# Optimization experiments

Measured on AMD Instinct MI355X. Metric: run time of the kernel, lower is better.

Reference implementation:

```python
import jax, jax.numpy as jnp
import numpy as np

HEADS1, HID = 2, 128
OUT_FEATS = 256
K, M = 8, 128


def _gat_conv(x, src, dst, W, a_src, a_dst, bias, heads, out_dim, concat, neg_slope):
    """PyG-style GATConv: linear -> per-edge leakyrelu attention -> dst-softmax -> scatter-sum."""
    N = x.shape[0]
    h = (x @ W.T).reshape(N, heads, out_dim)          # [N, H, D]
    alpha_src = jnp.sum(h * a_src, axis=-1)            # [N, H]
    alpha_dst = jnp.sum(h * a_dst, axis=-1)            # [N, H]
    e = jax.nn.leaky_relu(alpha_src[src] + alpha_dst[dst], neg_slope)  # [E, H]
    # numerically stable segment softmax over incoming edges per destination
    m = jax.ops.segment_max(e, dst, num_segments=N)    # [N, H]
    e = jnp.exp(e - m[dst])
    s = jax.ops.segment_sum(e, dst, num_segments=N)    # [N, H]
    alpha = e / s[dst]                                  # [E, H]
    msg = h[src] * alpha[:, :, None]                    # [E, H, D]
    out = jax.ops.segment_sum(msg, dst, num_segments=N)  # [N, H, D]
    out = out.reshape(N, heads * out_dim) if concat else out.mean(axis=1)
    return out + bias


def setup_inputs() -> dict:
    key = jax.random.key(0)
    ks = jax.random.split(key, 14)
    N, E, IN = 50000, 800000, 256
    x = jax.random.normal(ks[0], (N, IN), dtype=jnp.float32)
    edge_index = jax.random.randint(ks[1], (2, E), 0, N, dtype=jnp.int64)
    sc = 0.1
    return {
        "x": x,
        "edge_index": edge_index,
        "W1": jax.random.normal(ks[2], (HEADS1 * HID, IN), dtype=jnp.float32) * sc,
        "a_src1": jax.random.normal(ks[3], (HEADS1, HID), dtype=jnp.float32) * sc,
        "a_dst1": jax.random.normal(ks[4], (HEADS1, HID), dtype=jnp.float32) * sc,
        "b1": jax.random.normal(ks[5], (HEADS1 * HID,), dtype=jnp.float32) * sc,
        "W2": jax.random.normal(ks[6], (OUT_FEATS, HEADS1 * HID), dtype=jnp.float32) * sc,
        "a_src2": jax.random.normal(ks[7], (1, OUT_FEATS), dtype=jnp.float32) * sc,
        "a_dst2": jax.random.normal(ks[8], (1, OUT_FEATS), dtype=jnp.float32) * sc,
        "b2": jax.random.normal(ks[9], (OUT_FEATS,), dtype=jnp.float32) * sc,
        "g": jax.random.normal(ks[10], (OUT_FEATS, K * M), dtype=jnp.float32) * sc,
        "mu": jax.random.normal(ks[11], (K, M), dtype=jnp.float32) * sc,
    }


def reference(x, edge_index, W1, a_src1, a_dst1, b1, W2, a_src2, a_dst2, b2, g, mu):
    N = x.shape[0]
    loops = jnp.arange(N, dtype=edge_index.dtype)  # PyG GATConv adds self-loops by default
    src = jnp.concatenate([edge_index[0], loops])
    dst = jnp.concatenate([edge_index[1], loops])
    h = _gat_conv(x, src, dst, W1, a_src1, a_dst1, b1, HEADS1, HID, True, 0.2)
    h = jax.nn.leaky_relu(h, 0.01)  # F.leaky_relu default slope
    h = _gat_conv(h, src, dst, W2, a_src2, a_dst2, b2, 1, OUT_FEATS, False, 0.2)
    out = (h @ g).reshape(N, K, M)                      # [N, K, M]
    # cosine similarity against mu along M (torch eps=1e-8)
    num = jnp.einsum('nkm,km->nk', out, mu)
    denom = jnp.maximum(
        jnp.linalg.norm(out, axis=-1) * jnp.linalg.norm(mu, axis=-1)[None, :], 1e-8
    )
    return num / denom  # [N, K]
```

## Files before the change

kernel.cpp:

```cpp
#include <hip/hip_runtime.h>
#include <math.h>

typedef short s16x8 __attribute__((ext_vector_type(8)));
typedef float f32x4 __attribute__((ext_vector_type(4)));

__device__ __forceinline__ float lrelu(float x, float s) { return x > 0.0f ? x : s * x; }

__device__ __forceinline__ unsigned short f2bf(float f) {
  unsigned int u = __float_as_uint(f);
  u = (u + 0x7FFFu + ((u >> 16) & 1u)) >> 16;
  return (unsigned short)u;
}
__device__ __forceinline__ float bf2f(unsigned short h) {
  return __uint_as_float(((unsigned int)h) << 16);
}

__device__ __forceinline__ void gload_lds16(void* lds, const void* g) {
  __builtin_amdgcn_global_load_lds(
      (const __attribute__((address_space(1))) unsigned int*)g,
      (__attribute__((address_space(3))) unsigned int*)lds, 16, 0, 0);
}

__global__ void deg_kernel(const int* __restrict__ dst, int* __restrict__ deg, int E) {
  int e = blockIdx.x * blockDim.x + threadIdx.x;
  if (e < E) atomicAdd(&deg[dst[e]], 1);
}

__global__ __launch_bounds__(256) void bsum_kernel(const int* __restrict__ deg,
                                                   int* __restrict__ bsum, int N) {
  int t = blockIdx.x * 256 + threadIdx.x;
  int v = (t < N) ? deg[t] : 0;
  #pragma unroll
  for (int off = 1; off < 64; off <<= 1) v += __shfl_xor(v, off, 64);
  __shared__ int ws[4];
  if ((threadIdx.x & 63) == 0) ws[threadIdx.x >> 6] = v;
  __syncthreads();
  if (threadIdx.x == 0) bsum[blockIdx.x] = ws[0] + ws[1] + ws[2] + ws[3];
}

__global__ __launch_bounds__(256) void bscan_kernel(const int* __restrict__ bsum,
                                                    int* __restrict__ boff, int nb,
                                                    int* __restrict__ rowptr_total) {
  __shared__ int s[256];
  int t = threadIdx.x;
  int v = (t < nb) ? bsum[t] : 0;
  s[t] = v;
  __syncthreads();
  for (int off = 1; off < 256; off <<= 1) {
    int u = (t >= off) ? s[t - off] : 0;
    __syncthreads();
    s[t] += u;
    __syncthreads();
  }
  if (t < nb) boff[t] = s[t] - v;
  if (t == nb - 1) *rowptr_total = s[t];
}

__global__ __launch_bounds__(256) void bwrite_kernel(const int* __restrict__ deg,
                                                     const int* __restrict__ boff,
                                                     int* __restrict__ rowptr,
                                                     int* __restrict__ cursor, int N) {
  __shared__ int s[256];
  int t = blockIdx.x * 256 + threadIdx.x;
  int v = (t < N) ? deg[t] : 0;
  s[threadIdx.x] = v;
  __syncthreads();
  for (int off = 1; off < 256; off <<= 1) {
    int u = (threadIdx.x >= off) ? s[threadIdx.x - off] : 0;
    __syncthreads();
    s[threadIdx.x] += u;
    __syncthreads();
  }
  if (t < N) {
    int ex = boff[blockIdx.x] + s[threadIdx.x] - v;
    rowptr[t] = ex;
    cursor[t] = ex;
  }
}

__global__ void fill_kernel(const int* __restrict__ src, const int* __restrict__ dst,
                            int* __restrict__ cursor, int* __restrict__ colsrc, int E) {
  int e = blockIdx.x * blockDim.x + threadIdx.x;
  if (e < E) {
    int d = dst[e];
    int pos = atomicAdd(&cursor[d], 1);
    colsrc[pos] = src[e];
  }
}

__global__ void cvt_rows_kernel(const float* __restrict__ src, unsigned short* __restrict__ dst,
                                int nrows, int prows) {
  int t = blockIdx.x * blockDim.x + threadIdx.x;
  int row = t >> 6;
  int c = (t & 63) * 4;
  if (row >= prows) return;
  float4 v = make_float4(0.f, 0.f, 0.f, 0.f);
  if (row < nrows) v = *(const float4*)&src[(size_t)row * 256 + c];
  ushort4 o;
  o.x = f2bf(v.x); o.y = f2bf(v.y); o.z = f2bf(v.z); o.w = f2bf(v.w);
  *(ushort4*)&dst[(size_t)row * 256 + c] = o;
}

__global__ void cvt_gT_kernel(const float* __restrict__ g, unsigned short* __restrict__ gT) {
  int idx = blockIdx.x * blockDim.x + threadIdx.x;
  int k = idx >> 10, n = idx & 1023;
  gT[(size_t)n * 256 + k] = f2bf(g[idx]);
}

template<int EPI, int AH>
__global__ __launch_bounds__(256, 2) void gemm_bf16(
    const unsigned short* __restrict__ A, const unsigned short* __restrict__ B,
    unsigned short* __restrict__ Cb,
    const float* __restrict__ avs, const float* __restrict__ avd,
    float* __restrict__ asrcO, float* __restrict__ adstO,
    const float* __restrict__ mu, const float* __restrict__ nmu,
    float* __restrict__ outcos, int M)
{
  __shared__ unsigned short As[128 * 64];
  __shared__ unsigned short Bs[128 * 64];
  const int t = threadIdx.x;
  const int w = t >> 6;
  const int l = t & 63;
  const int m0 = blockIdx.x * 128;
  const int n0 = blockIdx.y * 128;

  f32x4 acc[2][8];
  #pragma unroll
  for (int i = 0; i < 2; ++i)
    #pragma unroll
    for (int j = 0; j < 8; ++j) acc[i][j] = (f32x4){0.f, 0.f, 0.f, 0.f};

  const unsigned char* Ab = (const unsigned char*)A;
  const unsigned char* Bb = (const unsigned char*)B;
  unsigned char* AsB = (unsigned char*)As;
  unsigned char* BsB = (unsigned char*)Bs;

  const int srow = l >> 3;
  const int gchk = (l & 7) ^ srow;

  for (int kb = 0; kb < 256; kb += 64) {
    #pragma unroll
    for (int i = 0; i < 4; ++i) {
      int seg = w * 4 + i;
      int row = seg * 8 + srow;
      gload_lds16(AsB + seg * 1024,
                  Ab + (size_t)(m0 + row) * 512 + kb * 2 + gchk * 16);
      gload_lds16(BsB + seg * 1024,
                  Bb + (size_t)(n0 + row) * 512 + kb * 2 + gchk * 16);
    }
    asm volatile("s_waitcnt vmcnt(0)" ::: "memory");
    __syncthreads();

    const int rl = l & 15;
    const int kc = l >> 4;
    #pragma unroll
    for (int ks = 0; ks < 2; ++ks) {
      s16x8 af[2], bfr[8];
      #pragma unroll
      for (int mf = 0; mf < 2; ++mf) {
        int r = w * 32 + mf * 16 + rl;
        int slot = (ks * 4 + kc) ^ (r & 7);
        af[mf] = *(const s16x8*)&As[r * 64 + slot * 8];
      }
      #pragma unroll
      for (int nf = 0; nf < 8; ++nf) {
        int r = nf * 16 + rl;
        int slot = (ks * 4 + kc) ^ (r & 7);
        bfr[nf] = *(const s16x8*)&Bs[r * 64 + slot * 8];
      }
      #pragma unroll
      for (int mf = 0; mf < 2; ++mf)
        #pragma unroll
        for (int nf = 0; nf < 8; ++nf)
          acc[mf][nf] = __builtin_amdgcn_mfma_f32_16x16x32_bf16(af[mf], bfr[nf], acc[mf][nf], 0, 0, 0);
    }
    __syncthreads();
  }

  if (EPI == 0) {
    #pragma unroll
    for (int mf = 0; mf < 2; ++mf)
      #pragma unroll
      for (int nf = 0; nf < 8; ++nf)
        #pragma unroll
        for (int j = 0; j < 4; ++j) {
          int r = m0 + w * 32 + mf * 16 + (l >> 4) * 4 + j;
          int c = n0 + nf * 16 + (l & 15);
          Cb[(size_t)r * 256 + c] = f2bf(acc[mf][nf][j]);
        }
    if (AH > 0) {
      float avS[8], avD[8];
      #pragma unroll
      for (int nf = 0; nf < 8; ++nf) {
        avS[nf] = avs[n0 + nf * 16 + (l & 15)];
        avD[nf] = avd[n0 + nf * 16 + (l & 15)];
      }
      #pragma unroll
      for (int mf = 0; mf < 2; ++mf)
        #pragma unroll
        for (int j = 0; j < 4; ++j) {
          float ds = 0.f, dd = 0.f;
          #pragma unroll
          for (int nf = 0; nf < 8; ++nf) {
            float o = acc[mf][nf][j];
            ds = fmaf(o, avS[nf], ds);
            dd = fmaf(o, avD[nf], dd);
          }
          #pragma unroll
          for (int off = 1; off < 16; off <<= 1) {
            ds += __shfl_xor(ds, off, 64);
            dd += __shfl_xor(dd, off, 64);
          }
          if ((l & 15) == 0) {
            int r = m0 + w * 32 + mf * 16 + (l >> 4) * 4 + j;
            if (r < M) {
              if (AH == 2) {
                asrcO[(size_t)r * 2 + blockIdx.y] = ds;
                adstO[(size_t)r * 2 + blockIdx.y] = dd;
              } else {
                atomicAdd(&asrcO[r], ds);
                atomicAdd(&adstO[r], dd);
              }
            }
          }
        }
    }
  } else {
    const int kchunk = blockIdx.y;
    float nm = nmu[kchunk];
    float mv[8];
    #pragma unroll
    for (int nf = 0; nf < 8; ++nf) mv[nf] = mu[kchunk * 128 + nf * 16 + (l & 15)];
    #pragma unroll
    for (int mf = 0; mf < 2; ++mf)
      #pragma unroll
      for (int j = 0; j < 4; ++j) {
        float num = 0.f, ss = 0.f;
        #pragma unroll
        for (int nf = 0; nf < 8; ++nf) {
          float o = acc[mf][nf][j];
          num = fmaf(o, mv[nf], num);
          ss  = fmaf(o, o, ss);
        }
        #pragma unroll
        for (int off = 1; off < 16; off <<= 1) {
          num += __shfl_xor(num, off, 64);
          ss  += __shfl_xor(ss, off, 64);
        }
        if ((l & 15) == 0) {
          int r = m0 + w * 32 + mf * 16 + (l >> 4) * 4 + j;
          if (r < M) outcos[(size_t)r * 8 + kchunk] = num / fmaxf(sqrtf(ss) * nm, 1e-8f);
        }
      }
  }
}

template<int H, bool OUT_LRELU>
__global__ __launch_bounds__(256) void agg_kernel(
    const unsigned short* __restrict__ hin, const float* __restrict__ asrc,
    const float* __restrict__ adst, const int* __restrict__ rowptr,
    const int* __restrict__ colsrc, const float* __restrict__ bias,
    unsigned short* __restrict__ outp, int N)
{
  int wid  = threadIdx.x >> 6;
  int lane = threadIdx.x & 63;
  int n = blockIdx.x * 4 + wid;
  if (n >= N) return;
  const int half = lane >> 5;
  const int fl   = lane & 31;
  const int head = (H == 2) ? (fl >> 4) : 0;

  int beg = rowptr[n], end = rowptr[n + 1];

  float ad0 = adst[(size_t)n * H + 0];
  float ad1 = (H == 2) ? adst[(size_t)n * 2 + 1] : 0.f;
  float m0 = lrelu(asrc[(size_t)n * H + 0] + ad0, 0.2f);
  float m1 = (H == 2) ? lrelu(asrc[(size_t)n * 2 + 1] + ad1, 0.2f) : 0.f;
  float s0 = 1.f, s1 = 1.f;

  float acc[8];
  {
    s16x8 hv = *(const s16x8*)&hin[(size_t)n * 256 + fl * 8];
    #pragma unroll
    for (int k = 0; k < 8; ++k)
      acc[k] = (half == 0) ? bf2f((unsigned short)hv[k]) : 0.f;
  }

  for (int cbeg = beg; cbeg < end; cbeg += 64) {
    int cnt = end - cbeg; if (cnt > 64) cnt = 64;
    int src_i = 0;
    float e0 = -1e30f, e1 = -1e30f;
    if (lane < cnt) {
      src_i = colsrc[cbeg + lane];
      if (H == 2) {
        float2 av = *(const float2*)&asrc[(size_t)src_i * 2];
        e0 = lrelu(av.x + ad0, 0.2f);
        e1 = lrelu(av.y + ad1, 0.2f);
      } else {
        e0 = lrelu(asrc[src_i] + ad0, 0.2f);
      }
    }
    float c0 = e0, c1 = e1;
    #pragma unroll
    for (int off = 32; off >= 1; off >>= 1) {
      c0 = fmaxf(c0, __shfl_xor(c0, off, 64));
      if (H == 2) c1 = fmaxf(c1, __shfl_xor(c1, off, 64));
    }
    float nm0 = fmaxf(m0, c0);
    float r0 = __expf(m0 - nm0); m0 = nm0;
    float r1 = 1.f;
    if (H == 2) { float nm1 = fmaxf(m1, c1); r1 = __expf(m1 - nm1); m1 = nm1; }
    s0 *= r0; if (H == 2) s1 *= r1;
    float rh = (H == 2 && head) ? r1 : r0;
    #pragma unroll
    for (int k = 0; k < 8; ++k) acc[k] *= rh;
    float p0 = (lane < cnt) ? __expf(e0 - m0) : 0.f;
    float p1 = (H == 2 && lane < cnt) ? __expf(e1 - m1) : 0.f;
    float t0 = p0, t1 = p1;
    #pragma unroll
    for (int off = 32; off >= 1; off >>= 1) {
      t0 += __shfl_xor(t0, off, 64);
      if (H == 2) t1 += __shfl_xor(t1, off, 64);
    }
    s0 += t0; if (H == 2) s1 += t1;

    int npair = (cnt + 1) >> 1;
    int pi = 0;
    for (; pi + 2 <= npair; pi += 2) {
      int ia = pi * 2, ib = pi * 2 + 2;
      int sa0 = __shfl(src_i, ia, 64),     sa1 = __shfl(src_i, ia + 1, 64);
      int sb0 = __shfl(src_i, ib, 64),     sb1 = __shfl(src_i, ib + 1, 64);
      float qa00 = __shfl(p0, ia, 64),     qa01 = __shfl(p0, ia + 1, 64);
      float qb00 = __shfl(p0, ib, 64),     qb01 = __shfl(p0, ib + 1, 64);
      float wA, wB;
      if (H == 2) {
        float qa10 = __shfl(p1, ia, 64), qa11 = __shfl(p1, ia + 1, 64);
        float qb10 = __shfl(p1, ib, 64), qb11 = __shfl(p1, ib + 1, 64);
        wA = head ? (half ? qa11 : qa10) : (half ? qa01 : qa00);
        wB = head ? (half ? qb11 : qb10) : (half ? qb01 : qb00);
      } else {
        wA = half ? qa01 : qa00;
        wB = half ? qb01 : qb00;
      }
      int sjA = half ? sa1 : sa0;
      int sjB = half ? sb1 : sb0;
      s16x8 vA = *(const s16x8*)&hin[(size_t)sjA * 256 + fl * 8];
      s16x8 vB = *(const s16x8*)&hin[(size_t)sjB * 256 + fl * 8];
      #pragma unroll
      for (int k = 0; k < 8; ++k) acc[k] = fmaf(bf2f((unsigned short)vA[k]), wA, acc[k]);
      #pragma unroll
      for (int k = 0; k < 8; ++k) acc[k] = fmaf(bf2f((unsigned short)vB[k]), wB, acc[k]);
    }
    for (; pi < npair; ++pi) {
      int ia = pi * 2;
      int sa0 = __shfl(src_i, ia, 64), sa1 = __shfl(src_i, ia + 1, 64);
      float qa00 = __shfl(p0, ia, 64), qa01 = __shfl(p0, ia + 1, 64);
      float wA;
      if (H == 2) {
        float qa10 = __shfl(p1, ia, 64), qa11 = __shfl(p1, ia + 1, 64);
        wA = head ? (half ? qa11 : qa10) : (half ? qa01 : qa00);
      } else {
        wA = half ? qa01 : qa00;
      }
      int sjA = half ? sa1 : sa0;
      s16x8 vA = *(const s16x8*)&hin[(size_t)sjA * 256 + fl * 8];
      #pragma unroll
      for (int k = 0; k < 8; ++k) acc[k] = fmaf(bf2f((unsigned short)vA[k]), wA, acc[k]);
    }
  }

  float sh = (H == 2 && head) ? s1 : s0;
  float inv = 1.0f / sh;
  #pragma unroll
  for (int k = 0; k < 8; ++k) acc[k] += __shfl_xor(acc[k], 32, 64);
  if (half == 0) {
    float bv[8];
    *(float4*)&bv[0] = *(const float4*)&bias[fl * 8];
    *(float4*)&bv[4] = *(const float4*)&bias[fl * 8 + 4];
    s16x8 o;
    #pragma unroll
    for (int k = 0; k < 8; ++k) {
      float v = acc[k] * inv + bv[k];
      if (OUT_LRELU) v = lrelu(v, 0.01f);
      o[k] = (short)f2bf(v);
    }
    *(s16x8*)&outp[(size_t)n * 256 + fl * 8] = o;
  }
}

__global__ __launch_bounds__(64) void munorm_kernel(const float* __restrict__ mu,
                                                    float* __restrict__ norm_mu) {
  int lane = threadIdx.x;
  for (int k = 0; k < 8; ++k) {
    float v0 = mu[k * 128 + lane];
    float v1 = mu[k * 128 + 64 + lane];
    float s = v0 * v0 + v1 * v1;
    #pragma unroll
    for (int off = 1; off < 64; off <<= 1) s += __shfl_xor(s, off, 64);
    if (lane == 0) norm_mu[k] = sqrtf(s);
  }
}

extern "C" void kernel_launch(void* const* d_in, const int* in_sizes, int n_in,
                              void* d_out, int out_size, void* d_ws, size_t ws_size,
                              hipStream_t stream) {
  const float* x      = (const float*)d_in[0];
  const int*   ei     = (const int*)  d_in[1];
  const float* W1     = (const float*)d_in[2];
  const float* a_src1 = (const float*)d_in[3];
  const float* a_dst1 = (const float*)d_in[4];
  const float* b1     = (const float*)d_in[5];
  const float* W2     = (const float*)d_in[6];
  const float* a_src2 = (const float*)d_in[7];
  const float* a_dst2 = (const float*)d_in[8];
  const float* b2     = (const float*)d_in[9];
  const float* g      = (const float*)d_in[10];
  const float* mu     = (const float*)d_in[11];

  const int N  = in_sizes[0] / 256;
  const int E  = in_sizes[1] / 2;
  const int Mp = ((N + 127) / 128) * 128;
  const int nb = (N + 255) / 256;
  const int* src = ei;
  const int* dst = ei + E;

  unsigned short* us = (unsigned short*)d_ws;
  size_t off = 0;
  unsigned short* xb  = us + off; off += (size_t)Mp * 256;
  unsigned short* h1b = us + off; off += (size_t)Mp * 256;
  unsigned short* o1b = us + off; off += (size_t)Mp * 256;
  unsigned short* h2b = us + off; off += (size_t)Mp * 256;
  unsigned short* o2b = xb;
  float* f = (float*)(us + off);
  size_t fo = 0;
  float* asrc1 = f + fo; fo += (size_t)N * 2;
  float* adst1 = f + fo; fo += (size_t)N * 2;
  float* asrc2 = f + fo; fo += N;
  float* adst2 = f + fo; fo += N;
  float* nmu   = f + fo; fo += 8;
  int* deg    = (int*)(f + fo);
  int* rowptr = deg + N;
  int* cursor = rowptr + N + 1;
  int* colsrc = cursor + N;
  int* bsum   = colsrc + E;
  int* boff   = bsum + 256;
  unsigned short* w1b = (unsigned short*)(boff + 256);
  unsigned short* w2b = w1b + 256 * 256;
  unsigned short* gTb = w2b + 256 * 256;

  hipMemsetAsync(deg, 0, (size_t)N * sizeof(int), stream);
  hipMemsetAsync(asrc2, 0, (size_t)N * 2 * sizeof(float), stream);
  deg_kernel<<<(E + 255) / 256, 256, 0, stream>>>(dst, deg, E);
  bsum_kernel<<<nb, 256, 0, stream>>>(deg, bsum, N);
  bscan_kernel<<<1, 256, 0, stream>>>(bsum, boff, nb, rowptr + N);
  bwrite_kernel<<<nb, 256, 0, stream>>>(deg, boff, rowptr, cursor, N);
  fill_kernel<<<(E + 255) / 256, 256, 0, stream>>>(src, dst, cursor, colsrc, E);

  cvt_rows_kernel<<<Mp / 4, 256, 0, stream>>>(x, xb, N, Mp);
  cvt_rows_kernel<<<64, 256, 0, stream>>>(W1, w1b, 256, 256);
  cvt_rows_kernel<<<64, 256, 0, stream>>>(W2, w2b, 256, 256);
  cvt_gT_kernel<<<1024, 256, 0, stream>>>(g, gTb);
  munorm_kernel<<<1, 64, 0, stream>>>(mu, nmu);

  const int gm = Mp / 128;

  gemm_bf16<0, 2><<<dim3(gm, 2), 256, 0, stream>>>(xb, w1b, h1b,
      a_src1, a_dst1, asrc1, adst1, nullptr, nullptr, nullptr, N);
  agg_kernel<2, true><<<(N + 3) / 4, 256, 0, stream>>>(h1b, asrc1, adst1, rowptr, colsrc, b1, o1b, N);

  gemm_bf16<0, 1><<<dim3(gm, 2), 256, 0, stream>>>(o1b, w2b, h2b,
      a_src2, a_dst2, asrc2, adst2, nullptr, nullptr, nullptr, N);
  agg_kernel<1, false><<<(N + 3) / 4, 256, 0, stream>>>(h2b, asrc2, adst2, rowptr, colsrc, b2, o2b, N);

  gemm_bf16<1, 0><<<dim3(gm, 8), 256, 0, stream>>>(o2b, gTb, nullptr,
      nullptr, nullptr, nullptr, nullptr, mu, nmu, (float*)d_out, N);
}
```

Baseline: 413.7 us.

## Remap GEMM blocks per XCD for L2 reuse and unroll aggregation gathers by four

```diff
diff --git a/kernel.cpp b/kernel.cpp
--- a/kernel.cpp
+++ b/kernel.cpp
@@ -107,7 +107,7 @@
   gT[(size_t)n * 256 + k] = f2bf(g[idx]);
 }
 
-template<int EPI, int AH>
+template<int EPI, int AH, int NY>
 __global__ __launch_bounds__(256, 2) void gemm_bf16(
     const unsigned short* __restrict__ A, const unsigned short* __restrict__ B,
     unsigned short* __restrict__ Cb,
@@ -118,17 +118,25 @@
 {
   __shared__ unsigned short As[128 * 64];
   __shared__ unsigned short Bs[128 * 64];
+  const int gm = (M + 127) >> 7;
+  const int id = blockIdx.x;
+  const int xcd = id & 7;
+  const int tt = id >> 3;
+  const int j  = tt & (NY - 1);
+  const int xg = tt / NY;
+  const int xt = xg * 8 + xcd;
+  if (xt >= gm) return;
   const int t = threadIdx.x;
   const int w = t >> 6;
   const int l = t & 63;
-  const int m0 = blockIdx.x * 128;
-  const int n0 = blockIdx.y * 128;
+  const int m0 = xt * 128;
+  const int n0 = j * 128;
 
   f32x4 acc[2][8];
   #pragma unroll
   for (int i = 0; i < 2; ++i)
     #pragma unroll
-    for (int j = 0; j < 8; ++j) acc[i][j] = (f32x4){0.f, 0.f, 0.f, 0.f};
+    for (int jj = 0; jj < 8; ++jj) acc[i][jj] = (f32x4){0.f, 0.f, 0.f, 0.f};
 
   const unsigned char* Ab = (const unsigned char*)A;
   const unsigned char* Bb = (const unsigned char*)B;
@@ -183,10 +191,10 @@
       #pragma unroll
       for (int nf = 0; nf < 8; ++nf)
         #pragma unroll
-        for (int j = 0; j < 4; ++j) {
-          int r = m0 + w * 32 + mf * 16 + (l >> 4) * 4 + j;
+        for (int jj = 0; jj < 4; ++jj) {
+          int r = m0 + w * 32 + mf * 16 + (l >> 4) * 4 + jj;
           int c = n0 + nf * 16 + (l & 15);
-          Cb[(size_t)r * 256 + c] = f2bf(acc[mf][nf][j]);
+          Cb[(size_t)r * 256 + c] = f2bf(acc[mf][nf][jj]);
         }
     if (AH > 0) {
       float avS[8], avD[8];
@@ -198,11 +206,11 @@
       #pragma unroll
       for (int mf = 0; mf < 2; ++mf)
         #pragma unroll
-        for (int j = 0; j < 4; ++j) {
+        for (int jj = 0; jj < 4; ++jj) {
           float ds = 0.f, dd = 0.f;
           #pragma unroll
           for (int nf = 0; nf < 8; ++nf) {
-            float o = acc[mf][nf][j];
+            float o = acc[mf][nf][jj];
             ds = fmaf(o, avS[nf], ds);
             dd = fmaf(o, avD[nf], dd);
           }
@@ -212,11 +220,11 @@
             dd += __shfl_xor(dd, off, 64);
           }
           if ((l & 15) == 0) {
-            int r = m0 + w * 32 + mf * 16 + (l >> 4) * 4 + j;
+            int r = m0 + w * 32 + mf * 16 + (l >> 4) * 4 + jj;
             if (r < M) {
               if (AH == 2) {
-                asrcO[(size_t)r * 2 + blockIdx.y] = ds;
-                adstO[(size_t)r * 2 + blockIdx.y] = dd;
+                asrcO[(size_t)r * 2 + j] = ds;
+                adstO[(size_t)r * 2 + j] = dd;
               } else {
                 atomicAdd(&asrcO[r], ds);
                 atomicAdd(&adstO[r], dd);
@@ -226,7 +234,7 @@
         }
     }
   } else {
-    const int kchunk = blockIdx.y;
+    const int kchunk = j;
     float nm = nmu[kchunk];
     float mv[8];
     #pragma unroll
@@ -234,11 +242,11 @@
     #pragma unroll
     for (int mf = 0; mf < 2; ++mf)
       #pragma unroll
-      for (int j = 0; j < 4; ++j) {
+      for (int jj = 0; jj < 4; ++jj) {
         float num = 0.f, ss = 0.f;
         #pragma unroll
         for (int nf = 0; nf < 8; ++nf) {
-          float o = acc[mf][nf][j];
+          float o = acc[mf][nf][jj];
           num = fmaf(o, mv[nf], num);
           ss  = fmaf(o, o, ss);
         }
@@ -248,7 +256,7 @@
           ss  += __shfl_xor(ss, off, 64);
         }
         if ((l & 15) == 0) {
-          int r = m0 + w * 32 + mf * 16 + (l >> 4) * 4 + j;
+          int r = m0 + w * 32 + mf * 16 + (l >> 4) * 4 + jj;
           if (r < M) outcos[(size_t)r * 8 + kchunk] = num / fmaxf(sqrtf(ss) * nm, 1e-8f);
         }
       }
@@ -325,47 +333,33 @@
     s0 += t0; if (H == 2) s1 += t1;
 
     int npair = (cnt + 1) >> 1;
-    int pi = 0;
-    for (; pi + 2 <= npair; pi += 2) {
-      int ia = pi * 2, ib = pi * 2 + 2;
-      int sa0 = __shfl(src_i, ia, 64),     sa1 = __shfl(src_i, ia + 1, 64);
-      int sb0 = __shfl(src_i, ib, 64),     sb1 = __shfl(src_i, ib + 1, 64);
-      float qa00 = __shfl(p0, ia, 64),     qa01 = __shfl(p0, ia + 1, 64);
-      float qb00 = __shfl(p0, ib, 64),     qb01 = __shfl(p0, ib + 1, 64);
-      float wA, wB;
-      if (H == 2) {
-        float qa10 = __shfl(p1, ia, 64), qa11 = __shfl(p1, ia + 1, 64);
-        float qb10 = __shfl(p1, ib, 64), qb11 = __shfl(p1, ib + 1, 64);
-        wA = head ? (half ? qa11 : qa10) : (half ? qa01 : qa00);
-        wB = head ? (half ? qb11 : qb10) : (half ? qb01 : qb00);
-      } else {
-        wA = half ? qa01 : qa00;
-        wB = half ? qb01 : qb00;
-      }
-      int sjA = half ? sa1 : sa0;
-      int sjB = half ? sb1 : sb0;
-      s16x8 vA = *(const s16x8*)&hin[(size_t)sjA * 256 + fl * 8];
-      s16x8 vB = *(const s16x8*)&hin[(size_t)sjB * 256 + fl * 8];
-      #pragma unroll
-      for (int k = 0; k < 8; ++k) acc[k] = fmaf(bf2f((unsigned short)vA[k]), wA, acc[k]);
-      #pragma unroll
-      for (int k = 0; k < 8; ++k) acc[k] = fmaf(bf2f((unsigned short)vB[k]), wB, acc[k]);
-    }
-    for (; pi < npair; ++pi) {
-      int ia = pi * 2;
-      int sa0 = __shfl(src_i, ia, 64), sa1 = __shfl(src_i, ia + 1, 64);
-      float qa00 = __shfl(p0, ia, 64), qa01 = __shfl(p0, ia + 1, 64);
-      float wA;
-      if (H == 2) {
-        float qa10 = __shfl(p1, ia, 64), qa11 = __shfl(p1, ia + 1, 64);
-        wA = head ? (half ? qa11 : qa10) : (half ? qa01 : qa00);
-      } else {
-        wA = half ? qa01 : qa00;
-      }
-      int sjA = half ? sa1 : sa0;
-      s16x8 vA = *(const s16x8*)&hin[(size_t)sjA * 256 + fl * 8];
-      #pragma unroll
-      for (int k = 0; k < 8; ++k) acc[k] = fmaf(bf2f((unsigned short)vA[k]), wA, acc[k]);
+    int npr = (npair + 3) & ~3;
+    for (int pi = 0; pi < npr; pi += 4) {
+      int sj[4]; float wv[4];
+      #pragma unroll
+      for (int u = 0; u < 4; ++u) {
+        int e = (pi + u) * 2 + half;
+        sj[u] = __shfl(src_i, e, 64);
+        float q0 = __shfl(p0, e, 64);
+        if (H == 2) {
+          float q1 = __shfl(p1, e, 64);
+          wv[u] = head ? q1 : q0;
+        } else {
+          wv[u] = q0;
+        }
+      }
+      s16x8 v0 = *(const s16x8*)&hin[(size_t)sj[0] * 256 + fl * 8];
+      s16x8 v1 = *(const s16x8*)&hin[(size_t)sj[1] * 256 + fl * 8];
+      s16x8 v2 = *(const s16x8*)&hin[(size_t)sj[2] * 256 + fl * 8];
+      s16x8 v3 = *(const s16x8*)&hin[(size_t)sj[3] * 256 + fl * 8];
+      #pragma unroll
+      for (int k = 0; k < 8; ++k) acc[k] = fmaf(bf2f((unsigned short)v0[k]), wv[0], acc[k]);
+      #pragma unroll
+      for (int k = 0; k < 8; ++k) acc[k] = fmaf(bf2f((unsigned short)v1[k]), wv[1], acc[k]);
+      #pragma unroll
+      for (int k = 0; k < 8; ++k) acc[k] = fmaf(bf2f((unsigned short)v2[k]), wv[2], acc[k]);
+      #pragma unroll
+      for (int k = 0; k < 8; ++k) acc[k] = fmaf(bf2f((unsigned short)v3[k]), wv[3], acc[k]);
     }
   }
 
@@ -462,16 +456,19 @@
   cvt_gT_kernel<<<1024, 256, 0, stream>>>(g, gTb);
   munorm_kernel<<<1, 64, 0, stream>>>(mu, nmu);
 
-  const int gm = Mp / 128;
-
-  gemm_bf16<0, 2><<<dim3(gm, 2), 256, 0, stream>>>(xb, w1b, h1b,
+  const int gm  = Mp / 128;
+  const int nxg = (gm + 7) / 8;
+  const int g2  = nxg * 8 * 2;
+  const int g8  = nxg * 8 * 8;
+
+  gemm_bf16<0, 2, 2><<<g2, 256, 0, stream>>>(xb, w1b, h1b,
       a_src1, a_dst1, asrc1, adst1, nullptr, nullptr, nullptr, N);
   agg_kernel<2, true><<<(N + 3) / 4, 256, 0, stream>>>(h1b, asrc1, adst1, rowptr, colsrc, b1, o1b, N);
 
-  gemm_bf16<0, 1><<<dim3(gm, 2), 256, 0, stream>>>(o1b, w2b, h2b,
+  gemm_bf16<0, 1, 2><<<g2, 256, 0, stream>>>(o1b, w2b, h2b,
       a_src2, a_dst2, asrc2, adst2, nullptr, nullptr, nullptr, N);
   agg_kernel<1, false><<<(N + 3) / 4, 256, 0, stream>>>(h2b, asrc2, adst2, rowptr, colsrc, b2, o2b, N);
 
-  gemm_bf16<1, 0><<<dim3(gm, 8), 256, 0, stream>>>(o2b, gTb, nullptr,
+  gemm_bf16<1, 0, 8><<<g8, 256, 0, stream>>>(o2b, gTb, nullptr,
       nullptr, nullptr, nullptr, nullptr, mu, nmu, (float*)d_out, N);
 }
```

Measured after the change: 419.0 us. About the same (+1.3%).

## Map full wavefront to one source row per edge in GAT aggregation

Applied to the files above, without the earlier changes.

```diff
diff --git a/kernel.cpp b/kernel.cpp
--- a/kernel.cpp
+++ b/kernel.cpp
@@ -13,6 +13,9 @@
 }
 __device__ __forceinline__ float bf2f(unsigned short h) {
   return __uint_as_float(((unsigned int)h) << 16);
+}
+__device__ __forceinline__ float bcastf(float v, int l) {
+  return __uint_as_float((unsigned)__builtin_amdgcn_readlane((int)__float_as_uint(v), l));
 }
 
 __device__ __forceinline__ void gload_lds16(void* lds, const void* g) {
@@ -266,9 +269,7 @@
   int lane = threadIdx.x & 63;
   int n = blockIdx.x * 4 + wid;
   if (n >= N) return;
-  const int half = lane >> 5;
-  const int fl   = lane & 31;
-  const int head = (H == 2) ? (fl >> 4) : 0;
+  const int head = (H == 2) ? (lane >> 5) : 0;
 
   int beg = rowptr[n], end = rowptr[n + 1];
 
@@ -278,12 +279,11 @@
   float m1 = (H == 2) ? lrelu(asrc[(size_t)n * 2 + 1] + ad1, 0.2f) : 0.f;
   float s0 = 1.f, s1 = 1.f;
 
-  float acc[8];
+  float acc[4];
   {
-    s16x8 hv = *(const s16x8*)&hin[(size_t)n * 256 + fl * 8];
-    #pragma unroll
-    for (int k = 0; k < 8; ++k)
-      acc[k] = (half == 0) ? bf2f((unsigned short)hv[k]) : 0.f;
+    ushort4 hv = *(const ushort4*)&hin[(size_t)n * 256 + lane * 4];
+    acc[0] = bf2f(hv.x); acc[1] = bf2f(hv.y);
+    acc[2] = bf2f(hv.z); acc[3] = bf2f(hv.w);
   }
 
   for (int cbeg = beg; cbeg < end; cbeg += 64) {
@@ -313,7 +313,7 @@
     s0 *= r0; if (H == 2) s1 *= r1;
     float rh = (H == 2 && head) ? r1 : r0;
     #pragma unroll
-    for (int k = 0; k < 8; ++k) acc[k] *= rh;
+    for (int k = 0; k < 4; ++k) acc[k] *= rh;
     float p0 = (lane < cnt) ? __expf(e0 - m0) : 0.f;
     float p1 = (H == 2 && lane < cnt) ? __expf(e1 - m1) : 0.f;
     float t0 = p0, t1 = p1;
@@ -324,68 +324,43 @@
     }
     s0 += t0; if (H == 2) s1 += t1;
 
-    int npair = (cnt + 1) >> 1;
-    int pi = 0;
-    for (; pi + 2 <= npair; pi += 2) {
-      int ia = pi * 2, ib = pi * 2 + 2;
-      int sa0 = __shfl(src_i, ia, 64),     sa1 = __shfl(src_i, ia + 1, 64);
-      int sb0 = __shfl(src_i, ib, 64),     sb1 = __shfl(src_i, ib + 1, 64);
-      float qa00 = __shfl(p0, ia, 64),     qa01 = __shfl(p0, ia + 1, 64);
-      float qb00 = __shfl(p0, ib, 64),     qb01 = __shfl(p0, ib + 1, 64);
-      float wA, wB;
-      if (H == 2) {
-        float qa10 = __shfl(p1, ia, 64), qa11 = __shfl(p1, ia + 1, 64);
-        float qb10 = __shfl(p1, ib, 64), qb11 = __shfl(p1, ib + 1, 64);
-        wA = head ? (half ? qa11 : qa10) : (half ? qa01 : qa00);
-        wB = head ? (half ? qb11 : qb10) : (half ? qb01 : qb00);
-      } else {
-        wA = half ? qa01 : qa00;
-        wB = half ? qb01 : qb00;
-      }
-      int sjA = half ? sa1 : sa0;
-      int sjB = half ? sb1 : sb0;
-      s16x8 vA = *(const s16x8*)&hin[(size_t)sjA * 256 + fl * 8];
-      s16x8 vB = *(const s16x8*)&hin[(size_t)sjB * 256 + fl * 8];
-      #pragma unroll
-      for (int k = 0; k < 8; ++k) acc[k] = fmaf(bf2f((unsigned short)vA[k]), wA, acc[k]);
-      #pragma unroll
-      for (int k = 0; k < 8; ++k) acc[k] = fmaf(bf2f((unsigned short)vB[k]), wB, acc[k]);
-    }
-    for (; pi < npair; ++pi) {
-      int ia = pi * 2;
-      int sa0 = __shfl(src_i, ia, 64), sa1 = __shfl(src_i, ia + 1, 64);
-      float qa00 = __shfl(p0, ia, 64), qa01 = __shfl(p0, ia + 1, 64);
-      float wA;
-      if (H == 2) {
-        float qa10 = __shfl(p1, ia, 64), qa11 = __shfl(p1, ia + 1, 64);
-        wA = head ? (half ? qa11 : qa10) : (half ? qa01 : qa00);
-      } else {
-        wA = half ? qa01 : qa00;
-      }
-      int sjA = half ? sa1 : sa0;
-      s16x8 vA = *(const s16x8*)&hin[(size_t)sjA * 256 + fl * 8];
-      #pragma unroll
-      for (int k = 0; k < 8; ++k) acc[k] = fmaf(bf2f((unsigned short)vA[k]), wA, acc[k]);
+    int ne4 = (cnt + 3) & ~3;
+    for (int e = 0; e < ne4; e += 4) {
+      ushort4 v[4]; float aw[4];
+      #pragma unroll
+      for (int u = 0; u < 4; ++u) {
+        int sidx = __builtin_amdgcn_readlane(src_i, e + u);
+        float a0 = bcastf(p0, e + u);
+        if (H == 2) {
+          float a1 = bcastf(p1, e + u);
+          aw[u] = head ? a1 : a0;
+        } else {
+          aw[u] = a0;
+        }
+        v[u] = *(const ushort4*)&hin[(size_t)sidx * 256 + lane * 4];
+      }
+      #pragma unroll
+      for (int u = 0; u < 4; ++u) {
+        acc[0] = fmaf(bf2f(v[u].x), aw[u], acc[0]);
+        acc[1] = fmaf(bf2f(v[u].y), aw[u], acc[1]);
+        acc[2] = fmaf(bf2f(v[u].z), aw[u], acc[2]);
+        acc[3] = fmaf(bf2f(v[u].w), aw[u], acc[3]);
+      }
     }
   }
 
   float sh = (H == 2 && head) ? s1 : s0;
   float inv = 1.0f / sh;
-  #pragma unroll
-  for (int k = 0; k < 8; ++k) acc[k] += __shfl_xor(acc[k], 32, 64);
-  if (half == 0) {
-    float bv[8];
-    *(float4*)&bv[0] = *(const float4*)&bias[fl * 8];
-    *(float4*)&bv[4] = *(const float4*)&bias[fl * 8 + 4];
-    s16x8 o;
-    #pragma unroll
-    for (int k = 0; k < 8; ++k) {
-      float v = acc[k] * inv + bv[k];
-      if (OUT_LRELU) v = lrelu(v, 0.01f);
-      o[k] = (short)f2bf(v);
-    }
-    *(s16x8*)&outp[(size_t)n * 256 + fl * 8] = o;
-  }
+  float4 bv = *(const float4*)&bias[lane * 4];
+  float o0 = acc[0] * inv + bv.x, o1 = acc[1] * inv + bv.y;
+  float o2 = acc[2] * inv + bv.z, o3 = acc[3] * inv + bv.w;
+  if (OUT_LRELU) {
+    o0 = lrelu(o0, 0.01f); o1 = lrelu(o1, 0.01f);
+    o2 = lrelu(o2, 0.01f); o3 = lrelu(o3, 0.01f);
+  }
+  ushort4 o;
+  o.x = f2bf(o0); o.y = f2bf(o1); o.z = f2bf(o2); o.w = f2bf(o3);
+  *(ushort4*)&outp[(size_t)n * 256 + lane * 4] = o;
 }
 
 __global__ __launch_bounds__(64) void munorm_kernel(const float* __restrict__ mu,
```

New measurement: 416.7 us. Within noise of the previous version (+0.7%).
